# Kernel optimization log

Measured on AMD Instinct MI355X. Metric: run time of the kernel, lower is better.

## Reference

```python
import jax, jax.numpy as jnp
import numpy as np

MODEL_DIM = 1024
NUM_HEADS = 16
HEAD_DIM = MODEL_DIM // NUM_HEADS


def setup_inputs() -> dict:
    key = jax.random.key(0)
    ks = jax.random.split(key, 9)
    B, S, D = 2, 2048, MODEL_DIM
    scale = 1.0 / np.sqrt(D)
    X = jax.random.normal(ks[0], (B, S, D), dtype=jnp.float32)
    Wq = jax.random.normal(ks[1], (D, D), dtype=jnp.float32) * scale
    bq = jax.random.normal(ks[2], (D,), dtype=jnp.float32) * 0.01
    Wk = jax.random.normal(ks[3], (D, D), dtype=jnp.float32) * scale
    bk = jax.random.normal(ks[4], (D,), dtype=jnp.float32) * 0.01
    Wv = jax.random.normal(ks[5], (D, D), dtype=jnp.float32) * scale
    bv = jax.random.normal(ks[6], (D,), dtype=jnp.float32) * 0.01
    Wo = jax.random.normal(ks[7], (D, D), dtype=jnp.float32) * scale
    bo = jax.random.normal(ks[8], (D,), dtype=jnp.float32) * 0.01
    return {"X": X, "Wq": Wq, "bq": bq, "Wk": Wk, "bk": bk,
            "Wv": Wv, "bv": bv, "Wo": Wo, "bo": bo}


def reference(X, Wq, bq, Wk, bk, Wv, bv, Wo, bo):
    B, S, D = X.shape
    H, Hd = NUM_HEADS, HEAD_DIM
    # QKV projections (torch Linear: x @ W.T + b; here W stored as (in, out))
    q = (X @ Wq + bq).reshape(B, S, H, Hd)
    k = (X @ Wk + bk).reshape(B, S, H, Hd)
    v = (X @ Wv + bv).reshape(B, S, H, Hd)
    # scores [B, H, S, S]
    score = jnp.einsum('bqhd,bkhd->bhqk', q, k) / jnp.sqrt(jnp.float32(Hd))
    causal = jnp.tril(jnp.ones((S, S), dtype=bool))
    score = jnp.where(causal[None, None], score, -jnp.inf)
    attn = jax.nn.softmax(score, axis=-1)
    out = jnp.einsum('bhqk,bkhd->bqhd', attn, v).reshape(B, S, D)
    return out @ Wo + bo
```

## Files before the change

### kernel.cpp

```cpp
#include <hip/hip_runtime.h>
#include <hip/hip_bf16.h>


#define D_MODEL 1024
#define SEQ     2048
#define NHEADS  16
#define HDIM    64
#define MROWS   4096
#define QSCALE  0.18033688011112042f

typedef __attribute__((ext_vector_type(8))) short short8;
typedef __attribute__((ext_vector_type(8))) _Float16 h8;
typedef __attribute__((ext_vector_type(4))) _Float16 h4;
typedef __attribute__((ext_vector_type(2))) __fp16 fp16x2;
typedef __attribute__((ext_vector_type(4))) float f32x4;

__device__ __forceinline__ ushort f2h(float x) {
    union { _Float16 h; ushort u; } c; c.h = (_Float16)x; return c.u;
}

__device__ __forceinline__ float ex2(float x) {
    float r;
    asm("v_exp_f32 %0, %1" : "=v"(r) : "v"(x));
    return r;
}

__device__ __forceinline__ h4 pack4(float p0, float p1, float p2, float p3) {
    union { fp16x2 h[2]; h4 v; } u;
    u.h[0] = __builtin_amdgcn_cvt_pkrtz(p0, p1);
    u.h[1] = __builtin_amdgcn_cvt_pkrtz(p2, p3);
    return u.v;
}

__device__ __forceinline__ unsigned pack2u(float p0, float p1) {
    union { fp16x2 h; unsigned u; } w;
    w.h = __builtin_amdgcn_cvt_pkrtz(p0, p1);
    return w.u;
}

#define GLDS(gp, lp) \
    __builtin_amdgcn_global_load_lds( \
        (const __attribute__((address_space(1))) void*)(gp), \
        (__attribute__((address_space(3))) void*)(lp), 16, 0, 0)

__device__ __forceinline__ const h8* lds_chunk(const ushort* base, int r, int c) {
    return (const h8*)(base + (((r << 3) + (c ^ (r & 7))) << 3));
}

__global__ __launch_bounds__(256) void prep(
    const float* __restrict__ W0, const float* __restrict__ W1,
    const float* __restrict__ W2, const float* __restrict__ W3,
    const float* __restrict__ X,
    ushort* __restrict__ Wt, ushort* __restrict__ Xh) {
    const int tid = threadIdx.x;
    const int z = blockIdx.z;
    if (z < 4) {
        __shared__ ushort Ts[64][72];
        const int n0 = blockIdx.x * 64, k0 = blockIdx.y * 64;
        const float* W = z == 0 ? W0 : (z == 1 ? W1 : (z == 2 ? W2 : W3));
        #pragma unroll
        for (int i = 0; i < 4; ++i) {
            int t = tid + 256 * i;
            int r = t >> 4, cg = t & 15;
            float4 f = *(const float4*)(W + (size_t)(k0 + r) * D_MODEL + n0 + cg * 4);
            Ts[cg * 4 + 0][r] = f2h(f.x);
            Ts[cg * 4 + 1][r] = f2h(f.y);
            Ts[cg * 4 + 2][r] = f2h(f.z);
            Ts[cg * 4 + 3][r] = f2h(f.w);
        }
        __syncthreads();
        #pragma unroll
        for (int i = 0; i < 2; ++i) {
            int t = tid + 256 * i;
            int nr = t >> 3, kg = t & 7;
            short8 v = *(const short8*)&Ts[nr][kg * 8];
            *(short8*)(Wt + ((size_t)z * D_MODEL + n0 + nr) * D_MODEL + k0 + kg * 8) = v;
        }
    } else {
        int base = (blockIdx.y * 16 + blockIdx.x) * 2048 + tid;
        #pragma unroll
        for (int i = 0; i < 8; ++i) {
            int idx = base + i * 256;
            float4 f0 = ((const float4*)X)[idx * 2];
            float4 f1 = ((const float4*)X)[idx * 2 + 1];
            short8 o;
            o[0] = f2h(f0.x); o[1] = f2h(f0.y); o[2] = f2h(f0.z); o[3] = f2h(f0.w);
            o[4] = f2h(f1.x); o[5] = f2h(f1.y); o[6] = f2h(f1.z); o[7] = f2h(f1.w);
            ((short8*)Xh)[idx] = o;
        }
    }
}

__device__ __forceinline__ void gemm_mainloop(
    const ushort* __restrict__ A, const ushort* __restrict__ Bt,
    ushort* Xs, ushort* Ws, int m0, int n0, int tid, f32x4 acc[4][4]) {
    const int wave = tid >> 6, lane = tid & 63;
    const int l16 = lane & 15, quad = lane >> 4;
    const int wm = wave >> 1, wn = wave & 1;

    const ushort* ag[4]; const ushort* bg[4]; ushort* al[4]; ushort* bl[4];
    #pragma unroll
    for (int i = 0; i < 4; ++i) {
        int slot = i * 256 + tid;
        int row = slot >> 3, cs = slot & 7;
        int c = cs ^ (row & 7);
        ag[i] = A + (size_t)(m0 + row) * D_MODEL + c * 8;
        bg[i] = Bt + (size_t)(n0 + row) * D_MODEL + c * 8;
        al[i] = Xs + (((i << 8) + (wave << 6)) << 3);
        bl[i] = Ws + (((i << 8) + (wave << 6)) << 3);
    }

    for (int k0 = 0; k0 < D_MODEL; k0 += 64) {
        #pragma unroll
        for (int i = 0; i < 4; ++i) { GLDS(ag[i], al[i]); ag[i] += 64; }
        #pragma unroll
        for (int i = 0; i < 4; ++i) { GLDS(bg[i], bl[i]); bg[i] += 64; }
        __syncthreads();
        #pragma unroll
        for (int kk = 0; kk < 2; ++kk) {
            h8 a[4], b[4];
            #pragma unroll
            for (int t = 0; t < 4; ++t) {
                a[t] = *lds_chunk(Xs, wm * 64 + t * 16 + l16, kk * 4 + quad);
                b[t] = *lds_chunk(Ws, wn * 64 + t * 16 + l16, kk * 4 + quad);
            }
            #pragma unroll
            for (int mt = 0; mt < 4; ++mt)
                #pragma unroll
                for (int nt = 0; nt < 4; ++nt)
                    acc[mt][nt] = __builtin_amdgcn_mfma_f32_16x16x32_f16(
                        b[nt], a[mt], acc[mt][nt], 0, 0, 0);
        }
        __syncthreads();
    }
}

__global__ __launch_bounds__(256) void qkv_gemm_h(
    const ushort* __restrict__ Xh, const ushort* __restrict__ Wt,
    const float* __restrict__ bq, const float* __restrict__ bk,
    const float* __restrict__ bv,
    ushort* __restrict__ Qh, ushort* __restrict__ Kh, ushort* __restrict__ Vh) {
    __shared__ ushort Xs[128 * 64];
    __shared__ ushort Ws[128 * 64];
    const int tid = threadIdx.x;
    const int id = blockIdx.x;
    const int xcd = id & 7, t = id >> 3;
    const int bm = (xcd & 3) * 8 + (t & 7);
    const int bn = (xcd >> 2) * 12 + (t >> 3);
    const int m0 = bm * 128, n0 = bn * 128;

    f32x4 acc[4][4];
    #pragma unroll
    for (int mt = 0; mt < 4; ++mt)
        #pragma unroll
        for (int nt = 0; nt < 4; ++nt) acc[mt][nt] = (f32x4){0.f, 0.f, 0.f, 0.f};

    gemm_mainloop(Xh, Wt, Xs, Ws, m0, n0, tid, acc);

    const int wave = tid >> 6, lane = tid & 63;
    const int l16 = lane & 15, quad = lane >> 4;
    const int wm = wave >> 1, wn = wave & 1;
    const int seg = n0 >> 10;
    const float* bias = seg == 0 ? bq : (seg == 1 ? bk : bv);
    ushort* dst = seg == 0 ? Qh : (seg == 1 ? Kh : Vh);
    const float sc = seg == 0 ? QSCALE : 1.0f;

    #pragma unroll
    for (int mt = 0; mt < 4; ++mt) {
        int m = m0 + wm * 64 + mt * 16 + l16;
        int bi = m >> 11, s = m & 2047;
        #pragma unroll
        for (int nt = 0; nt < 4; ++nt) {
            int nn = (n0 + wn * 64 + nt * 16 + quad * 4) & 1023;
            int h = nn >> 6, d = nn & 63;
            float4 bb = *(const float4*)(bias + nn);
            f32x4 v = acc[mt][nt];
            uint2 w;
            w.x = pack2u((v[0] + bb.x) * sc, (v[1] + bb.y) * sc);
            w.y = pack2u((v[2] + bb.z) * sc, (v[3] + bb.w) * sc);
            *(uint2*)(dst + ((size_t)(bi * NHEADS + h) * SEQ + s) * HDIM + d) = w;
        }
    }
}

__global__ __launch_bounds__(256) void out_gemm_h(
    const ushort* __restrict__ Ah, const ushort* __restrict__ Wot,
    const float* __restrict__ bo, float* __restrict__ Out) {
    __shared__ ushort Xs[128 * 64];
    __shared__ ushort Ws2[64 * 64];
    const int tid = threadIdx.x;
    const int id = blockIdx.x;
    const int xcd = id & 7, t = id >> 3;
    const int bm = (xcd & 3) * 8 + (t & 7);
    const int bn = (xcd >> 2) * 8 + (t >> 3);
    const int m0 = bm * 128, n0 = bn * 64;
    const int wave = tid >> 6, lane = tid & 63;
    const int l16 = lane & 15, quad = lane >> 4;

    f32x4 acc[2][4];
    #pragma unroll
    for (int mt = 0; mt < 2; ++mt)
        #pragma unroll
        for (int nt = 0; nt < 4; ++nt) acc[mt][nt] = (f32x4){0.f, 0.f, 0.f, 0.f};

    const ushort* ag[4]; const ushort* bg[2]; ushort* al[4]; ushort* bl[2];
    #pragma unroll
    for (int i = 0; i < 4; ++i) {
        int slot = i * 256 + tid;
        int row = slot >> 3, cs = slot & 7;
        int c = cs ^ (row & 7);
        ag[i] = Ah + (size_t)(m0 + row) * D_MODEL + c * 8;
        al[i] = Xs + (((i << 8) + (wave << 6)) << 3);
    }
    #pragma unroll
    for (int i = 0; i < 2; ++i) {
        int slot = i * 256 + tid;
        int row = slot >> 3, cs = slot & 7;
        int c = cs ^ (row & 7);
        bg[i] = Wot + (size_t)(n0 + row) * D_MODEL + c * 8;
        bl[i] = Ws2 + (((i << 8) + (wave << 6)) << 3);
    }

    for (int k0 = 0; k0 < D_MODEL; k0 += 64) {
        #pragma unroll
        for (int i = 0; i < 4; ++i) { GLDS(ag[i], al[i]); ag[i] += 64; }
        #pragma unroll
        for (int i = 0; i < 2; ++i) { GLDS(bg[i], bl[i]); bg[i] += 64; }
        __syncthreads();
        #pragma unroll
        for (int kk = 0; kk < 2; ++kk) {
            h8 a[2], b[4];
            #pragma unroll
            for (int mt = 0; mt < 2; ++mt)
                a[mt] = *lds_chunk(Xs, wave * 32 + mt * 16 + l16, kk * 4 + quad);
            #pragma unroll
            for (int nt = 0; nt < 4; ++nt)
                b[nt] = *lds_chunk(Ws2, nt * 16 + l16, kk * 4 + quad);
            #pragma unroll
            for (int mt = 0; mt < 2; ++mt)
                #pragma unroll
                for (int nt = 0; nt < 4; ++nt)
                    acc[mt][nt] = __builtin_amdgcn_mfma_f32_16x16x32_f16(
                        b[nt], a[mt], acc[mt][nt], 0, 0, 0);
        }
        __syncthreads();
    }

    #pragma unroll
    for (int mt = 0; mt < 2; ++mt) {
        int m = m0 + wave * 32 + mt * 16 + l16;
        #pragma unroll
        for (int nt = 0; nt < 4; ++nt) {
            int n = n0 + nt * 16 + quad * 4;
            float4 bb = *(const float4*)(bo + n);
            f32x4 v = acc[mt][nt];
            float4 o;
            o.x = v[0] + bb.x; o.y = v[1] + bb.y;
            o.z = v[2] + bb.z; o.w = v[3] + bb.w;
            *(float4*)(Out + (size_t)m * D_MODEL + n) = o;
        }
    }
}

__device__ __forceinline__ void attn_step(
    const h8 kf[4][2], const h4 vf[4][4], const h8* qfg,
    f32x4* oacc, float& l_r,
    int kt, int qtg, int qrow, int quad) {
    f32x4 s[4];
    #pragma unroll
    for (int nt = 0; nt < 4; ++nt) {
        f32x4 z = (f32x4){0.f, 0.f, 0.f, 0.f};
        z = __builtin_amdgcn_mfma_f32_16x16x32_f16(kf[nt][0], qfg[0], z, 0, 0, 0);
        z = __builtin_amdgcn_mfma_f32_16x16x32_f16(kf[nt][1], qfg[1], z, 0, 0, 0);
        s[nt] = z;
    }
    if (kt == qtg) {
        #pragma unroll
        for (int nt = 0; nt < 4; ++nt)
            #pragma unroll
            for (int r = 0; r < 4; ++r) {
                int key = kt * 64 + nt * 16 + quad * 4 + r;
                if (key > qrow) s[nt][r] = -1e30f;
            }
    }
    float pn[4];
    h4 pf[4];
    #pragma unroll
    for (int nt = 0; nt < 4; ++nt) {
        float p0 = ex2(s[nt][0] - 8.f);
        float p1 = ex2(s[nt][1] - 8.f);
        float p2 = ex2(s[nt][2] - 8.f);
        float p3 = ex2(s[nt][3] - 8.f);
        pn[nt] = (p0 + p1) + (p2 + p3);
        pf[nt] = pack4(p0, p1, p2, p3);
    }
    l_r += (pn[0] + pn[1]) + (pn[2] + pn[3]);

    #pragma unroll
    for (int dt = 0; dt < 4; ++dt)
        #pragma unroll
        for (int nt = 0; nt < 4; ++nt)
            oacc[dt] = __builtin_amdgcn_mfma_f32_16x16x16f16(
                vf[dt][nt], pf[nt], oacc[dt], 0, 0, 0);
}

__global__ __launch_bounds__(512, 4) void flash_attn_mfma(
    const ushort* __restrict__ Q, const ushort* __restrict__ K,
    const ushort* __restrict__ V, ushort* __restrict__ O) {
    __shared__ ushort Ks[2][64 * 64];
    __shared__ ushort Vt[2][64][72];
    __shared__ ushort Os[8][16][72];

    const int tid  = threadIdx.x;
    const int wave = tid >> 6;
    const int lane = tid & 63;
    const int l16  = lane & 15;
    const int quad = lane >> 4;
    const int wg   = wave & 3;
    const bool heavy = wave < 4;
    const int bh   = blockIdx.y;
    const int b    = bh >> 4, h = bh & 15;
    const int qt0  = blockIdx.x;
    const int qt1  = 31 - qt0;
    const int myqt = heavy ? qt1 : qt0;

    const ushort* Qb = Q + (size_t)bh * SEQ * HDIM;
    const ushort* Kb = K + (size_t)bh * SEQ * HDIM;
    const ushort* Vb = V + (size_t)bh * SEQ * HDIM;

    const int qrow = myqt * 64 + wg * 16 + l16;

    h8 qf[2];
    qf[0] = *(const h8*)(Qb + (size_t)qrow * HDIM + quad * 8);
    qf[1] = *(const h8*)(Qb + (size_t)qrow * HDIM + 32 + quad * 8);

    f32x4 oacc[4];
    #pragma unroll
    for (int dt = 0; dt < 4; ++dt) oacc[dt] = (f32x4){0.f, 0.f, 0.f, 0.f};
    float l_r = 0.f;

    const int vkp = tid & 31, vdg = (tid >> 5) & 7;
    uint4 va, vb4;

    if (heavy) {
        #pragma unroll
        for (int i = 0; i < 2; ++i) {
            int slot = i * 256 + tid;
            int row = slot >> 3, cs = slot & 7;
            int c = cs ^ (row & 7);
            GLDS(Kb + row * HDIM + c * 8,
                 &Ks[0][0] + (((i << 8) + (wave << 6)) << 3));
        }
    } else {
        const ushort* vap = Vb + (size_t)(2 * vkp) * HDIM + vdg * 8;
        va  = *(const uint4*)vap;
        vb4 = *(const uint4*)(vap + HDIM);
    }

    for (int kt = 0; kt <= qt1; ++kt) {
        const int cur = kt & 1;
        if (!heavy) {
            unsigned av[4] = {va.x, va.y, va.z, va.w};
            unsigned bv[4] = {vb4.x, vb4.y, vb4.z, vb4.w};
            #pragma unroll
            for (int j = 0; j < 4; ++j) {
                unsigned lo = (av[j] & 0xffffu) | (bv[j] << 16);
                unsigned hi = (av[j] >> 16) | (bv[j] & 0xffff0000u);
                ((unsigned*)&Vt[cur][vdg * 8 + 2 * j][0])[vkp] = lo;
                ((unsigned*)&Vt[cur][vdg * 8 + 2 * j + 1][0])[vkp] = hi;
            }
        }
        __syncthreads();

        if (kt < qt1) {
            if (heavy) {
                const ushort* Ktile = Kb + (size_t)(kt + 1) * 64 * HDIM;
                #pragma unroll
                for (int i = 0; i < 2; ++i) {
                    int slot = i * 256 + tid;
                    int row = slot >> 3, cs = slot & 7;
                    int c = cs ^ (row & 7);
                    GLDS(Ktile + row * HDIM + c * 8,
                         &Ks[1 - cur][0] + (((i << 8) + (wave << 6)) << 3));
                }
            } else {
                const ushort* vap =
                    Vb + (size_t)((kt + 1) * 64 + 2 * vkp) * HDIM + vdg * 8;
                va  = *(const uint4*)vap;
                vb4 = *(const uint4*)(vap + HDIM);
            }
        }

        if (heavy || kt <= qt0) {
            h8 kf[4][2];
            #pragma unroll
            for (int nt = 0; nt < 4; ++nt) {
                kf[nt][0] = *lds_chunk(&Ks[cur][0], nt * 16 + l16, quad);
                kf[nt][1] = *lds_chunk(&Ks[cur][0], nt * 16 + l16, 4 + quad);
            }
            h4 vf[4][4];
            #pragma unroll
            for (int dt = 0; dt < 4; ++dt)
                #pragma unroll
                for (int nt = 0; nt < 4; ++nt)
                    vf[dt][nt] =
                        *(const h4*)&Vt[cur][dt * 16 + l16][nt * 16 + quad * 4];

            attn_step(kf, vf, qf, oacc, l_r, kt, myqt, qrow, quad);
        }
    }

    {
        float l = l_r;
        l += __shfl_xor(l, 16);
        l += __shfl_xor(l, 32);
        float inv = 1.f / l;
        #pragma unroll
        for (int dt = 0; dt < 4; ++dt)
            #pragma unroll
            for (int r = 0; r < 4; r += 2) {
                unsigned w = pack2u(oacc[dt][r] * inv, oacc[dt][r + 1] * inv);
                *(unsigned*)&Os[wave][l16][dt * 16 + quad * 4 + r] = w;
            }
        asm volatile("s_waitcnt lgkmcnt(0)" ::: "memory");
        int qr = lane >> 2, dc = lane & 3;
        const ushort* src = &Os[wave][qr][dc * 16];
        short8 v0 = *(const short8*)src;
        short8 v1 = *(const short8*)(src + 8);
        int q = myqt * 64 + wg * 16 + qr;
        ushort* orow = O + (((size_t)b * SEQ + q) * NHEADS + h) * HDIM + dc * 16;
        *(short8*)orow = v0;
        *(short8*)(orow + 8) = v1;
    }
}

extern "C" void kernel_launch(void* const* d_in, const int* in_sizes, int n_in,
                              void* d_out, int out_size, void* d_ws, size_t ws_size,
                              hipStream_t stream)
{
    const float* X  = (const float*)d_in[0];
    const float* Wq = (const float*)d_in[1];
    const float* bq = (const float*)d_in[2];
    const float* Wk = (const float*)d_in[3];
    const float* bk = (const float*)d_in[4];
    const float* Wv = (const float*)d_in[5];
    const float* bv = (const float*)d_in[6];
    const float* Wo = (const float*)d_in[7];
    const float* bo = (const float*)d_in[8];
    float* out = (float*)d_out;

    const size_t MAT = (size_t)MROWS * D_MODEL;
    ushort* Xh = (ushort*)d_ws;
    ushort* Wt = Xh + MAT;
    ushort* Qh = Wt + (size_t)4 * D_MODEL * D_MODEL;
    ushort* Kh = Qh + MAT;
    ushort* Vh = Kh + MAT;
    ushort* Ah = Vh + MAT;

    prep<<<dim3(16, 16, 5), 256, 0, stream>>>(Wq, Wk, Wv, Wo, X, Wt, Xh);
    qkv_gemm_h<<<dim3(768), 256, 0, stream>>>(Xh, Wt, bq, bk, bv, Qh, Kh, Vh);
    flash_attn_mfma<<<dim3(16, 2 * NHEADS), 512, 0, stream>>>(Qh, Kh, Vh, Ah);
    out_gemm_h<<<dim3(512), 256, 0, stream>>>(
        Ah, Wt + (size_t)3 * D_MODEL * D_MODEL, bo, out);
}
```

Measured before the change: 187.8 us.

## Process both paired query tiles per wave, sharing K/V fragments from LDS

The flash attention block drops from 8 waves to 4, and each wave now computes both the heavy (qt1) and light (qt0) query tiles, reusing the same K and V register fragments for the two attn_step calls. The V transpose store uses a permuted column index so each lane can read its V fragment with two 128-bit LDS loads instead of four 64-bit ones. This halves the LDS fragment reads per query tile and removes the separate producer roles, at the cost of doubled accumulator registers per wave and fewer waves per block to hide latency. An extra lgkmcnt wait is added before the output stores because the Os staging buffer is reused across the two tiles.

New measurement: 190.3 us. About the same (+1.4%).

```diff
diff --git a/kernel.cpp b/kernel.cpp
--- a/kernel.cpp
+++ b/kernel.cpp
@@ -304,54 +304,54 @@
                 vf[dt][nt], pf[nt], oacc[dt], 0, 0, 0);
 }
 
-__global__ __launch_bounds__(512, 4) void flash_attn_mfma(
+__global__ __launch_bounds__(256, 2) void flash_attn_mfma(
     const ushort* __restrict__ Q, const ushort* __restrict__ K,
     const ushort* __restrict__ V, ushort* __restrict__ O) {
     __shared__ ushort Ks[2][64 * 64];
     __shared__ ushort Vt[2][64][72];
-    __shared__ ushort Os[8][16][72];
+    __shared__ ushort Os[4][16][72];
 
     const int tid  = threadIdx.x;
     const int wave = tid >> 6;
     const int lane = tid & 63;
     const int l16  = lane & 15;
     const int quad = lane >> 4;
-    const int wg   = wave & 3;
-    const bool heavy = wave < 4;
     const int bh   = blockIdx.y;
     const int b    = bh >> 4, h = bh & 15;
     const int qt0  = blockIdx.x;
     const int qt1  = 31 - qt0;
-    const int myqt = heavy ? qt1 : qt0;
 
     const ushort* Qb = Q + (size_t)bh * SEQ * HDIM;
     const ushort* Kb = K + (size_t)bh * SEQ * HDIM;
     const ushort* Vb = V + (size_t)bh * SEQ * HDIM;
 
-    const int qrow = myqt * 64 + wg * 16 + l16;
-
-    h8 qf[2];
-    qf[0] = *(const h8*)(Qb + (size_t)qrow * HDIM + quad * 8);
-    qf[1] = *(const h8*)(Qb + (size_t)qrow * HDIM + 32 + quad * 8);
-
-    f32x4 oacc[4];
-    #pragma unroll
-    for (int dt = 0; dt < 4; ++dt) oacc[dt] = (f32x4){0.f, 0.f, 0.f, 0.f};
-    float l_r = 0.f;
-
-    const int vkp = tid & 31, vdg = (tid >> 5) & 7;
+    const int qrow0 = qt0 * 64 + wave * 16 + l16;
+    const int qrow1 = qt1 * 64 + wave * 16 + l16;
+
+    h8 qf[2][2];
+    qf[0][0] = *(const h8*)(Qb + (size_t)qrow0 * HDIM + quad * 8);
+    qf[0][1] = *(const h8*)(Qb + (size_t)qrow0 * HDIM + 32 + quad * 8);
+    qf[1][0] = *(const h8*)(Qb + (size_t)qrow1 * HDIM + quad * 8);
+    qf[1][1] = *(const h8*)(Qb + (size_t)qrow1 * HDIM + 32 + quad * 8);
+
+    f32x4 oacc[2][4];
+    #pragma unroll
+    for (int g = 0; g < 2; ++g)
+        #pragma unroll
+        for (int dt = 0; dt < 4; ++dt) oacc[g][dt] = (f32x4){0.f, 0.f, 0.f, 0.f};
+    float l_r[2] = {0.f, 0.f};
+
+    const int vkp = tid & 31, vdg = tid >> 5;
+    const int pk2 = ((vkp >> 1) & 3) * 8 + (vkp >> 3) * 2 + (vkp & 1);
     uint4 va, vb4;
 
-    if (heavy) {
-        #pragma unroll
-        for (int i = 0; i < 2; ++i) {
-            int slot = i * 256 + tid;
-            int row = slot >> 3, cs = slot & 7;
-            int c = cs ^ (row & 7);
-            GLDS(Kb + row * HDIM + c * 8,
-                 &Ks[0][0] + (((i << 8) + (wave << 6)) << 3));
-        }
-    } else {
+    #pragma unroll
+    for (int i = 0; i < 2; ++i) {
+        int slot = i * 256 + tid;
+        GLDS(Kb + (slot >> 3) * HDIM + (((slot & 7) ^ ((slot >> 3) & 7)) * 8),
+             &Ks[0][0] + (((i << 8) + (wave << 6)) << 3));
+    }
+    {
         const ushort* vap = Vb + (size_t)(2 * vkp) * HDIM + vdg * 8;
         va  = *(const uint4*)vap;
         vb4 = *(const uint4*)(vap + HDIM);
@@ -359,59 +359,61 @@
 
     for (int kt = 0; kt <= qt1; ++kt) {
         const int cur = kt & 1;
-        if (!heavy) {
+        {
             unsigned av[4] = {va.x, va.y, va.z, va.w};
             unsigned bv[4] = {vb4.x, vb4.y, vb4.z, vb4.w};
             #pragma unroll
             for (int j = 0; j < 4; ++j) {
                 unsigned lo = (av[j] & 0xffffu) | (bv[j] << 16);
                 unsigned hi = (av[j] >> 16) | (bv[j] & 0xffff0000u);
-                ((unsigned*)&Vt[cur][vdg * 8 + 2 * j][0])[vkp] = lo;
-                ((unsigned*)&Vt[cur][vdg * 8 + 2 * j + 1][0])[vkp] = hi;
+                ((unsigned*)&Vt[cur][vdg * 8 + 2 * j][0])[pk2] = lo;
+                ((unsigned*)&Vt[cur][vdg * 8 + 2 * j + 1][0])[pk2] = hi;
             }
         }
         __syncthreads();
 
         if (kt < qt1) {
-            if (heavy) {
-                const ushort* Ktile = Kb + (size_t)(kt + 1) * 64 * HDIM;
-                #pragma unroll
-                for (int i = 0; i < 2; ++i) {
-                    int slot = i * 256 + tid;
-                    int row = slot >> 3, cs = slot & 7;
-                    int c = cs ^ (row & 7);
-                    GLDS(Ktile + row * HDIM + c * 8,
-                         &Ks[1 - cur][0] + (((i << 8) + (wave << 6)) << 3));
-                }
-            } else {
-                const ushort* vap =
-                    Vb + (size_t)((kt + 1) * 64 + 2 * vkp) * HDIM + vdg * 8;
-                va  = *(const uint4*)vap;
-                vb4 = *(const uint4*)(vap + HDIM);
+            const ushort* Ktile = Kb + (size_t)(kt + 1) * 64 * HDIM;
+            #pragma unroll
+            for (int i = 0; i < 2; ++i) {
+                int slot = i * 256 + tid;
+                GLDS(Ktile + (slot >> 3) * HDIM +
+                         (((slot & 7) ^ ((slot >> 3) & 7)) * 8),
+                     &Ks[1 - cur][0] + (((i << 8) + (wave << 6)) << 3));
             }
-        }
-
-        if (heavy || kt <= qt0) {
-            h8 kf[4][2];
-            #pragma unroll
-            for (int nt = 0; nt < 4; ++nt) {
-                kf[nt][0] = *lds_chunk(&Ks[cur][0], nt * 16 + l16, quad);
-                kf[nt][1] = *lds_chunk(&Ks[cur][0], nt * 16 + l16, 4 + quad);
-            }
-            h4 vf[4][4];
-            #pragma unroll
-            for (int dt = 0; dt < 4; ++dt)
-                #pragma unroll
-                for (int nt = 0; nt < 4; ++nt)
-                    vf[dt][nt] =
-                        *(const h4*)&Vt[cur][dt * 16 + l16][nt * 16 + quad * 4];
-
-            attn_step(kf, vf, qf, oacc, l_r, kt, myqt, qrow, quad);
-        }
-    }
-
-    {
-        float l = l_r;
+            const ushort* vap =
+                Vb + (size_t)((kt + 1) * 64 + 2 * vkp) * HDIM + vdg * 8;
+            va  = *(const uint4*)vap;
+            vb4 = *(const uint4*)(vap + HDIM);
+        }
+
+        h8 kf[4][2];
+        #pragma unroll
+        for (int nt = 0; nt < 4; ++nt) {
+            kf[nt][0] = *lds_chunk(&Ks[cur][0], nt * 16 + l16, quad);
+            kf[nt][1] = *lds_chunk(&Ks[cur][0], nt * 16 + l16, 4 + quad);
+        }
+        h4 vf[4][4];
+        #pragma unroll
+        for (int dt = 0; dt < 4; ++dt) {
+            const h8* p = (const h8*)&Vt[cur][dt * 16 + l16][quad * 16];
+            union { h8 v8; h4 v4[2]; } u0, u1;
+            u0.v8 = p[0];
+            u1.v8 = p[1];
+            vf[dt][0] = u0.v4[0];
+            vf[dt][1] = u0.v4[1];
+            vf[dt][2] = u1.v4[0];
+            vf[dt][3] = u1.v4[1];
+        }
+
+        attn_step(kf, vf, qf[1], oacc[1], l_r[1], kt, qt1, qrow1, quad);
+        if (kt <= qt0)
+            attn_step(kf, vf, qf[0], oacc[0], l_r[0], kt, qt0, qrow0, quad);
+    }
+
+    #pragma unroll
+    for (int g = 0; g < 2; ++g) {
+        float l = l_r[g];
         l += __shfl_xor(l, 16);
         l += __shfl_xor(l, 32);
         float inv = 1.f / l;
@@ -419,7 +421,7 @@
         for (int dt = 0; dt < 4; ++dt)
             #pragma unroll
             for (int r = 0; r < 4; r += 2) {
-                unsigned w = pack2u(oacc[dt][r] * inv, oacc[dt][r + 1] * inv);
+                unsigned w = pack2u(oacc[g][dt][r] * inv, oacc[g][dt][r + 1] * inv);
                 *(unsigned*)&Os[wave][l16][dt * 16 + quad * 4 + r] = w;
             }
         asm volatile("s_waitcnt lgkmcnt(0)" ::: "memory");
@@ -427,7 +429,8 @@
         const ushort* src = &Os[wave][qr][dc * 16];
         short8 v0 = *(const short8*)src;
         short8 v1 = *(const short8*)(src + 8);
-        int q = myqt * 64 + wg * 16 + qr;
+        asm volatile("s_waitcnt lgkmcnt(0)" ::: "memory");
+        int q = (g ? qt1 : qt0) * 64 + wave * 16 + qr;
         ushort* orow = O + (((size_t)b * SEQ + q) * NHEADS + h) * HDIM + dc * 16;
         *(short8*)orow = v0;
         *(short8*)(orow + 8) = v1;
@@ -459,7 +462,7 @@
 
     prep<<<dim3(16, 16, 5), 256, 0, stream>>>(Wq, Wk, Wv, Wo, X, Wt, Xh);
     qkv_gemm_h<<<dim3(768), 256, 0, stream>>>(Xh, Wt, bq, bk, bv, Qh, Kh, Vh);
-    flash_attn_mfma<<<dim3(16, 2 * NHEADS), 512, 0, stream>>>(Qh, Kh, Vh, Ah);
+    flash_attn_mfma<<<dim3(16, 2 * NHEADS), 256, 0, stream>>>(Qh, Kh, Vh, Ah);
     out_gemm_h<<<dim3(512), 256, 0, stream>>>(
         Ah, Wt + (size_t)3 * D_MODEL * D_MODEL, bo, out);
 }
```
